# Optimization experiments

Measured on AMD Instinct MI355X. Metric: run time of the kernel, lower is better.

Reference implementation:

```python
import jax, jax.numpy as jnp
import numpy as np

N = 50000      # nodes
E = 800000     # edges
D_IN = 128     # raw feature dim
H = 96         # hidden_channels
K = 8          # experts
L = 4          # num_layers
C = 40         # classes


def setup_inputs() -> dict:
    key = jax.random.key(0)
    ks = jax.random.split(key, 10)
    stdv = 1.0 / np.sqrt(H)
    inp = {
        'x': jax.random.normal(ks[0], (N, D_IN), dtype=jnp.float32),
        'edge_index': jax.random.randint(ks[1], (2, E), 0, N, dtype=jnp.int64),
        # fcs[0]: Linear(d, hidden); fcs[1]: Linear(hidden, c)
        'fc0_w': jax.random.normal(ks[2], (D_IN, H), dtype=jnp.float32) * 0.05,
        'fc0_b': jnp.zeros((H,), dtype=jnp.float32),
        'fc1_w': jax.random.normal(ks[3], (H, C), dtype=jnp.float32) * 0.05,
        'fc1_b': jnp.zeros((C,), dtype=jnp.float32),
        # context_enc (method='node'): per-layer Linear(hidden, K)
        'ctx_w': jax.random.normal(ks[4], (L, H, K), dtype=jnp.float32) * 0.05,
        'ctx_b': jnp.zeros((L, K), dtype=jnp.float32),
        # GraphMultiConvolution weights: [L, K, hidden, hidden], uniform(-stdv, stdv)
        'conv_w': jax.random.uniform(ks[5], (L, K, H, H), dtype=jnp.float32,
                                     minval=-stdv, maxval=stdv),
    }
    return inp


def reference(x, edge_index, fc0_w, fc0_b, fc1_w, fc1_b, ctx_w, ctx_b, conv_w):
    # eval-mode forward (training=False): no dropout, softmax routing
    row = edge_index[0]
    col = edge_index[1]
    h = jax.nn.relu(x @ fc0_w + fc0_b)                     # [N, H]
    for i in range(L):
        # routing logits and soft expert weights z: [N, K]
        z = jax.nn.softmax(h @ ctx_w[i] + ctx_b[i], axis=-1)
        # spmm aggregation: hi[r] = sum over edges (r, c) of h[c]
        hi = jax.ops.segment_sum(h[col], row, num_segments=N)  # [N, H]
        # K-expert batched matmul: [N, K, H]
        outs = jnp.einsum('nd,kdo->nko', hi, conv_w[i])
        # gumbel/softmax-weighted combine + residual
        out = jnp.einsum('nk,nko->no', z, outs) + h
        h = jax.nn.relu(out)
    return h @ fc1_w + fc1_b                               # [N, C]
```

## Files before the change

### kernel.cpp

```cpp
#include <hip/hip_runtime.h>

#define N_NODES 50000
#define N_EDGES 800000
#define DIN     128
#define H       96
#define K_EXP   8
#define L_LAYERS 4
#define C_OUT   40

#define GSZ 6250

typedef _Float16 f16;
typedef f16 f16x2 __attribute__((ext_vector_type(2)));
typedef f16 f16x4 __attribute__((ext_vector_type(4)));
typedef f16 f16x8 __attribute__((ext_vector_type(8)));
typedef float f32x4 __attribute__((ext_vector_type(4)));


#define CONV_TOT (L_LAYERS * K_EXP * H * H)
#define FC0_TOT  (DIN * H)
#define FC1_TOT  (48 * H)
#define CNT_BLOCKS ((N_EDGES + 255) / 256)
#define CVT_BLOCKS ((CONV_TOT + FC0_TOT + FC1_TOT + 255) / 256)

__global__ __launch_bounds__(256) void count_convert(const int* __restrict__ row,
                                                     int* __restrict__ deg,
                                                     int* __restrict__ p,
                                                     const float* __restrict__ conv_w,
                                                     const float* __restrict__ fc0_w,
                                                     const float* __restrict__ fc1_w,
                                                     f16* __restrict__ wfrag,
                                                     f16* __restrict__ fc0t,
                                                     f16* __restrict__ fc1t) {
    int tid = threadIdx.x;
    if ((int)blockIdx.x < CNT_BLOCKS) {
        int i = blockIdx.x * 256 + tid;
        if (i < N_EDGES) p[i] = atomicAdd(&deg[row[i]], 1);
    } else {
        int i = ((int)blockIdx.x - CNT_BLOCKS) * 256 + tid;
        if (i < CONV_TOT) {
            int o = i % H;
            int t = i / H;
            int d = t % H;
            int lk = t / H;
            int ct = o >> 4, lc = o & 15;
            int ks = d >> 5, quad = (d >> 3) & 3, j = d & 7;
            wfrag[(size_t)lk * 9216 + ct * 1536 + ks * 512 + (quad * 16 + lc) * 8 + j] =
                (f16)conv_w[i];
        } else if (i < CONV_TOT + FC0_TOT) {
            int j = i - CONV_TOT;
            int o = j % H, d = j / H;
            fc0t[o * DIN + d] = (f16)fc0_w[j];
        } else if (i < CONV_TOT + FC0_TOT + FC1_TOT) {
            int j = i - CONV_TOT - FC0_TOT;
            int o = j / H, d = j % H;
            fc1t[j] = (o < C_OUT) ? (f16)fc1_w[d * C_OUT + o] : (f16)0.f;
        }
    }
}

__global__ __launch_bounds__(1024) void scanA(const int* __restrict__ deg,
                                              int* __restrict__ rowptr,
                                              int* __restrict__ partial, int n) {
    __shared__ int wsum[16];
    int tid  = threadIdx.x;
    int lane = tid & 63, wid = tid >> 6;
    int idx = blockIdx.x * 1024 + tid;
    int v = (idx < n) ? deg[idx] : 0;
    int s = v;
    #pragma unroll
    for (int off = 1; off < 64; off <<= 1) {
        int t = __shfl_up(s, off, 64);
        if (lane >= off) s += t;
    }
    if (lane == 63) wsum[wid] = s;
    __syncthreads();
    if (wid == 0 && lane < 16) {
        int w = wsum[lane];
        #pragma unroll
        for (int off = 1; off < 16; off <<= 1) {
            int t = __shfl_up(w, off, 16);
            if (lane >= off) w += t;
        }
        wsum[lane] = w;
    }
    __syncthreads();
    int waveoff = (wid == 0) ? 0 : wsum[wid - 1];
    if (idx < n) rowptr[idx + 1] = waveoff + s;
    if (tid == 1023) partial[blockIdx.x] = waveoff + s;
}

__global__ __launch_bounds__(1024) void scanC(int* __restrict__ rowptr,
                                              const int* __restrict__ partial,
                                              int nb, int n) {
    __shared__ int boff_s;
    int tid = threadIdx.x;
    if (tid < 64) {
        int v = 0;
        for (int j = tid; j < (int)blockIdx.x; j += 64) v += partial[j];
        #pragma unroll
        for (int off = 32; off >= 1; off >>= 1) v += __shfl_xor(v, off, 64);
        if (tid == 0) boff_s = v;
    }
    __syncthreads();
    int boff = boff_s;
    int idx = blockIdx.x * 1024 + tid;
    if (idx == 0) rowptr[0] = 0;
    if (idx < n) rowptr[idx + 1] += boff;
}

__global__ __launch_bounds__(256) void scatter_store_xcd(const int* __restrict__ row,
                                                         const int* __restrict__ col,
                                                         const int* __restrict__ p,
                                                         const int* __restrict__ rowptr,
                                                         int* __restrict__ csr, int e) {
    int g = blockIdx.x & 7;
    int rlo = g * GSZ, rhi = rlo + GSZ;
    int stride = (gridDim.x >> 3) * 256;
    for (int i = (blockIdx.x >> 3) * 256 + threadIdx.x; i < e; i += stride) {
        int r = row[i];
        if (r >= rlo && r < rhi)
            csr[rowptr[r] + p[i]] = col[i];
    }
}


#define SPMM_BLOCKS ((N_NODES + 15) / 16)
#define CTX_BLOCKS  ((N_NODES + 255) / 256)

#define ACC8(v) { _Pragma("unroll") for (int q = 0; q < 8; q++) acc[q] += (float)(v)[q]; }

__global__ __launch_bounds__(256) void layer_pre(const f16* __restrict__ h16,
                                                 const int* __restrict__ rowptr,
                                                 const int* __restrict__ csr,
                                                 f16* __restrict__ hi16,
                                                 const float* __restrict__ cw,
                                                 const float* __restrict__ cb,
                                                 float* __restrict__ zt, int n) {
    __shared__ float ws[H * K_EXP];
    __shared__ float bs[K_EXP];
    int tid = threadIdx.x;
    if ((int)blockIdx.x < SPMM_BLOCKS) {
        int r  = blockIdx.x * 16 + (tid >> 4);
        int li = tid & 15;
        if (r >= n) return;
        bool act = li < 12;
        int j = rowptr[r], e = rowptr[r + 1];
        float acc[8] = {};
        const f16* hb = h16 + li * 8;

        int4 qa = *(const int4*)(csr + j);
        int4 qb = *(const int4*)(csr + j + 4);

        while (j + 8 <= e) {
            int4 na = *(const int4*)(csr + j + 8);
            int4 nb = *(const int4*)(csr + j + 12);
            f16x8 v0 = {}, v1 = {}, v2 = {}, v3 = {}, v4 = {}, v5 = {}, v6 = {}, v7 = {};
            if (act) {
                v0 = *(const f16x8*)(hb + (size_t)qa.x * H);
                v1 = *(const f16x8*)(hb + (size_t)qa.y * H);
                v2 = *(const f16x8*)(hb + (size_t)qa.z * H);
                v3 = *(const f16x8*)(hb + (size_t)qa.w * H);
                v4 = *(const f16x8*)(hb + (size_t)qb.x * H);
                v5 = *(const f16x8*)(hb + (size_t)qb.y * H);
                v6 = *(const f16x8*)(hb + (size_t)qb.z * H);
                v7 = *(const f16x8*)(hb + (size_t)qb.w * H);
            }
            ACC8(v0) ACC8(v1) ACC8(v2) ACC8(v3)
            ACC8(v4) ACC8(v5) ACC8(v6) ACC8(v7)
            j += 8; qa = na; qb = nb;
        }
        if (j + 4 <= e) {
            f16x8 v0 = {}, v1 = {}, v2 = {}, v3 = {};
            if (act) {
                v0 = *(const f16x8*)(hb + (size_t)qa.x * H);
                v1 = *(const f16x8*)(hb + (size_t)qa.y * H);
                v2 = *(const f16x8*)(hb + (size_t)qa.z * H);
                v3 = *(const f16x8*)(hb + (size_t)qa.w * H);
            }
            ACC8(v0) ACC8(v1) ACC8(v2) ACC8(v3)
            j += 4; qa = qb;
        }
        int rem = e - j;
        if (rem > 0) {
            f16x8 v0 = {}, v1 = {}, v2 = {};
            if (act) {
                v0 = *(const f16x8*)(hb + (size_t)qa.x * H);
                if (rem > 1) v1 = *(const f16x8*)(hb + (size_t)qa.y * H);
                if (rem > 2) v2 = *(const f16x8*)(hb + (size_t)qa.z * H);
            }
            ACC8(v0)
            if (rem > 1) ACC8(v1)
            if (rem > 2) ACC8(v2)
        }
        if (act) {
            f16x8 o;
            #pragma unroll
            for (int q = 0; q < 8; q++) o[q] = (f16)acc[q];
            *(f16x8*)(hi16 + (size_t)r * H + li * 8) = o;
        }
    } else {
        for (int t = tid; t < H * K_EXP; t += 256) ws[t] = cw[t];
        if (tid < K_EXP) bs[tid] = cb[tid];
        __syncthreads();
        int node = ((int)blockIdx.x - SPMM_BLOCKS) * 256 + tid;
        if (node >= n) return;
        float acc[K_EXP];
        #pragma unroll
        for (int k = 0; k < K_EXP; k++) acc[k] = bs[k];
        const f16* hr = h16 + (size_t)node * H;
        #pragma unroll 3
        for (int c8 = 0; c8 < 12; c8++) {
            f16x8 v = *(const f16x8*)(hr + c8 * 8);
            #pragma unroll
            for (int j = 0; j < 8; j++) {
                float hv = (float)v[j];
                int d = c8 * 8 + j;
                #pragma unroll
                for (int k = 0; k < K_EXP; k++) acc[k] += hv * ws[d * K_EXP + k];
            }
        }
        float mx = acc[0];
        #pragma unroll
        for (int k = 1; k < K_EXP; k++) mx = fmaxf(mx, acc[k]);
        float s = 0.f;
        #pragma unroll
        for (int k = 0; k < K_EXP; k++) { acc[k] = __expf(acc[k] - mx); s += acc[k]; }
        float inv = 1.f / s;
        #pragma unroll
        for (int k = 0; k < K_EXP; k++)
            zt[(size_t)k * N_NODES + node] = acc[k] * inv;
    }
}


#define FPAD 136

__global__ __launch_bounds__(256) void fc0_kernel(const float* __restrict__ x,
                                                  const f16* __restrict__ fc0t,
                                                  const float* __restrict__ b,
                                                  f16* __restrict__ h16, int n) {
    __shared__ f16 As[64 * FPAD];
    __shared__ f16 Ws[96 * FPAD];
    int tid = threadIdx.x;
    int l = tid & 63, w = tid >> 6;
    int quad = l >> 4, lc = l & 15;
    int row0 = blockIdx.x * 64;

    for (int t = tid; t < 2048; t += 256) {
        int m = t >> 5, c4 = (t & 31) * 4;
        int gr = row0 + m;
        float4 v = {0.f, 0.f, 0.f, 0.f};
        if (gr < n) v = *(const float4*)(x + (size_t)gr * DIN + c4);
        f16x4 h4 = {(f16)v.x, (f16)v.y, (f16)v.z, (f16)v.w};
        *(f16x4*)&As[m * FPAD + c4] = h4;
    }
    for (int t = tid; t < 1536; t += 256) {
        int o = t >> 4, c8 = (t & 15) * 8;
        *(f16x8*)&Ws[o * FPAD + c8] = *(const f16x8*)(fc0t + o * DIN + c8);
    }
    __syncthreads();

    f16x8 afr[4];
    #pragma unroll
    for (int ks = 0; ks < 4; ks++)
        afr[ks] = *(const f16x8*)&As[(16 * w + lc) * FPAD + ks * 32 + quad * 8];

    f32x4 acc[6] = {};
    #pragma unroll
    for (int ct = 0; ct < 6; ct++) {
        #pragma unroll
        for (int ks = 0; ks < 4; ks++) {
            f16x8 bfr = *(const f16x8*)&Ws[(ct * 16 + lc) * FPAD + ks * 32 + quad * 8];
            acc[ct] = __builtin_amdgcn_mfma_f32_16x16x32_f16(afr[ks], bfr, acc[ct], 0, 0, 0);
        }
    }

    int m0 = 16 * w + quad * 4;
    #pragma unroll
    for (int r = 0; r < 4; r++) {
        int gr = row0 + m0 + r;
        if (gr < n) {
            #pragma unroll
            for (int ct = 0; ct < 6; ct++) {
                int o = ct * 16 + lc;
                h16[(size_t)gr * H + o] = (f16)fmaxf(acc[ct][r] + b[o], 0.f);
            }
        }
    }
}


#define EG_STAGE 2
#define EG_HALFS (EG_STAGE * 9216)

__global__ __launch_bounds__(256) void expert_gemm(const f16* __restrict__ hi16,
                                                   const f16* __restrict__ hin16,
                                                   const f16* __restrict__ wfrag,
                                                   const float* __restrict__ zt,
                                                   f16* __restrict__ hout16, int n) {
    __shared__ f16 Wl[EG_HALFS];
    int tid = threadIdx.x;
    int l = tid & 63, w = tid >> 6;
    int quad = l >> 4, lc = l & 15;
    int brow = blockIdx.x * 128;
    int wrow0 = brow + w * 16;
    int wrow1 = wrow0 + 64;

    f16x8 afr0[3], afr1[3];
    #pragma unroll
    for (int ks = 0; ks < 3; ks++) {
        afr0[ks] = *(const f16x8*)(hi16 + (size_t)(wrow0 + lc) * H + ks * 32 + quad * 8);
        afr1[ks] = *(const f16x8*)(hi16 + (size_t)(wrow1 + lc) * H + ks * 32 + quad * 8);
    }

    f32x4 acc0[6] = {};
    f32x4 acc1[6] = {};

    for (int kb = 0; kb < K_EXP; kb += EG_STAGE) {
        __syncthreads();
        const f16* src = wfrag + (size_t)kb * 9216;
        for (int t = tid; t < EG_HALFS / 8; t += 256)
            *(f16x8*)&Wl[t * 8] = *(const f16x8*)(src + t * 8);
        __syncthreads();

        #pragma unroll
        for (int k2 = 0; k2 < EG_STAGE; k2++) {
            int k = kb + k2;
            f32x4 zf0 = *(const f32x4*)(zt + (size_t)k * N_NODES + wrow0 + quad * 4);
            f32x4 zf1 = *(const f32x4*)(zt + (size_t)k * N_NODES + wrow1 + quad * 4);
            #pragma unroll
            for (int ct = 0; ct < 6; ct++) {
                f16x8 b0 = *(const f16x8*)&Wl[k2 * 9216 + ct * 1536 + 0 * 512 + l * 8];
                f16x8 b1 = *(const f16x8*)&Wl[k2 * 9216 + ct * 1536 + 1 * 512 + l * 8];
                f16x8 b2 = *(const f16x8*)&Wl[k2 * 9216 + ct * 1536 + 2 * 512 + l * 8];
                f32x4 t0 = {};
                t0 = __builtin_amdgcn_mfma_f32_16x16x32_f16(afr0[0], b0, t0, 0, 0, 0);
                t0 = __builtin_amdgcn_mfma_f32_16x16x32_f16(afr0[1], b1, t0, 0, 0, 0);
                t0 = __builtin_amdgcn_mfma_f32_16x16x32_f16(afr0[2], b2, t0, 0, 0, 0);
                acc0[ct] += zf0 * t0;
                f32x4 t1 = {};
                t1 = __builtin_amdgcn_mfma_f32_16x16x32_f16(afr1[0], b0, t1, 0, 0, 0);
                t1 = __builtin_amdgcn_mfma_f32_16x16x32_f16(afr1[1], b1, t1, 0, 0, 0);
                t1 = __builtin_amdgcn_mfma_f32_16x16x32_f16(afr1[2], b2, t1, 0, 0, 0);
                acc1[ct] += zf1 * t1;
            }
        }
    }

    #pragma unroll
    for (int r = 0; r < 4; r++) {
        int gr0 = wrow0 + quad * 4 + r;
        if (gr0 < n) {
            #pragma unroll
            for (int ct = 0; ct < 6; ct++) {
                int o = ct * 16 + lc;
                float v = fmaxf(acc0[ct][r] + (float)hin16[(size_t)gr0 * H + o], 0.f);
                hout16[(size_t)gr0 * H + o] = (f16)v;
            }
        }
        int gr1 = wrow1 + quad * 4 + r;
        if (gr1 < n) {
            #pragma unroll
            for (int ct = 0; ct < 6; ct++) {
                int o = ct * 16 + lc;
                float v = fmaxf(acc1[ct][r] + (float)hin16[(size_t)gr1 * H + o], 0.f);
                hout16[(size_t)gr1 * H + o] = (f16)v;
            }
        }
    }
}


#define APAD 104

__global__ __launch_bounds__(256) void fc1_kernel(const f16* __restrict__ h16,
                                                  const f16* __restrict__ fc1t,
                                                  const float* __restrict__ b,
                                                  float* __restrict__ out, int n) {
    __shared__ f16 As[64 * APAD];
    __shared__ f16 Ws[48 * APAD];
    int tid = threadIdx.x;
    int l = tid & 63, w = tid >> 6;
    int quad = l >> 4, lc = l & 15;
    int row0 = blockIdx.x * 64;

    for (int t = tid; t < 768; t += 256) {
        int m = t / 12, c8 = (t % 12) * 8;
        int gr = row0 + m;
        f16x8 v = {};
        if (gr < n) v = *(const f16x8*)(h16 + (size_t)gr * H + c8);
        *(f16x8*)&As[m * APAD + c8] = v;
    }
    for (int t = tid; t < 576; t += 256) {
        int o = t / 12, c8 = (t % 12) * 8;
        *(f16x8*)&Ws[o * APAD + c8] = *(const f16x8*)(fc1t + o * H + c8);
    }
    __syncthreads();

    f16x8 afr[3];
    #pragma unroll
    for (int ks = 0; ks < 3; ks++)
        afr[ks] = *(const f16x8*)&As[(16 * w + lc) * APAD + ks * 32 + quad * 8];

    f32x4 acc[3] = {};
    #pragma unroll
    for (int ct = 0; ct < 3; ct++) {
        #pragma unroll
        for (int ks = 0; ks < 3; ks++) {
            f16x8 bfr = *(const f16x8*)&Ws[(ct * 16 + lc) * APAD + ks * 32 + quad * 8];
            acc[ct] = __builtin_amdgcn_mfma_f32_16x16x32_f16(afr[ks], bfr, acc[ct], 0, 0, 0);
        }
    }

    int m0 = 16 * w + quad * 4;
    #pragma unroll
    for (int r = 0; r < 4; r++) {
        int gr = row0 + m0 + r;
        if (gr < n) {
            #pragma unroll
            for (int ct = 0; ct < 3; ct++) {
                int o = ct * 16 + lc;
                if (o < C_OUT)
                    out[(size_t)gr * C_OUT + o] = acc[ct][r] + b[o];
            }
        }
    }
}


extern "C" void kernel_launch(void* const* d_in, const int* in_sizes, int n_in,
                              void* d_out, int out_size, void* d_ws, size_t ws_size,
                              hipStream_t stream) {
    const float* x      = (const float*)d_in[0];
    const int*   ei     = (const int*)d_in[1];
    const float* fc0_w  = (const float*)d_in[2];
    const float* fc0_b  = (const float*)d_in[3];
    const float* fc1_w  = (const float*)d_in[4];
    const float* fc1_b  = (const float*)d_in[5];
    const float* ctx_w  = (const float*)d_in[6];
    const float* ctx_b  = (const float*)d_in[7];
    const float* conv_w = (const float*)d_in[8];
    float* out = (float*)d_out;

    const size_t NH = (size_t)N_NODES * H;

    float* zbuf = (float*)d_ws;
    f16*   h16a = (f16*)(zbuf + (size_t)N_NODES * K_EXP);
    f16*   h16b = h16a + NH;
    f16*   hi16 = h16b + NH;
    f16*   wfrag= hi16 + NH;
    f16*   fc0t = wfrag + CONV_TOT;
    f16*   fc1t = fc0t + FC0_TOT;
    int* rowptr = (int*)(fc1t + FC1_TOT);
    int* deg    = rowptr + (N_NODES + 1);
    int* csr    = deg + N_NODES;
    int* prank  = csr + N_EDGES;
    int* partial  = prank + N_EDGES;

    const int* row = ei;
    const int* col = ei + N_EDGES;

    hipMemsetAsync(deg, 0, sizeof(int) * N_NODES, stream);

    count_convert<<<CNT_BLOCKS + CVT_BLOCKS, 256, 0, stream>>>(
        row, deg, prank, conv_w, fc0_w, fc1_w, wfrag, fc0t, fc1t);
    int nsb = (N_NODES + 1023) / 1024;
    scanA<<<nsb, 1024, 0, stream>>>(deg, rowptr, partial, N_NODES);
    scanC<<<nsb, 1024, 0, stream>>>(rowptr, partial, nsb, N_NODES);
    scatter_store_xcd<<<1024, 256, 0, stream>>>(row, col, prank, rowptr, csr, N_EDGES);

    int gemm_grid = (N_NODES + 63) / 64;
    fc0_kernel<<<gemm_grid, 256, 0, stream>>>(x, fc0t, fc0_b, h16a, N_NODES);

    int eg_grid = (N_NODES + 127) / 128;
    f16* hcur = h16a;
    f16* hnext = h16b;
    for (int i = 0; i < L_LAYERS; i++) {
        layer_pre<<<SPMM_BLOCKS + CTX_BLOCKS, 256, 0, stream>>>(
            hcur, rowptr, csr, hi16,
            ctx_w + (size_t)i * H * K_EXP, ctx_b + (size_t)i * K_EXP, zbuf, N_NODES);
        expert_gemm<<<eg_grid, 256, 0, stream>>>(
            hi16, hcur, wfrag + (size_t)i * K_EXP * H * H, zbuf, hnext, N_NODES);
        f16* t = hcur; hcur = hnext; hnext = t;
    }
    fc1_kernel<<<gemm_grid, 256, 0, stream>>>(hcur, fc1t, fc1_b, out, N_NODES);
}
```

Measured before the change: 369.7 us.

## Fuse CSR scatter with fc0, fold routing weights into A operand of expert MFMA

```diff
diff --git a/kernel.cpp b/kernel.cpp
--- a/kernel.cpp
+++ b/kernel.cpp
@@ -7,8 +7,6 @@
 #define K_EXP   8
 #define L_LAYERS 4
 #define C_OUT   40
-
-#define GSZ 6250
 
 typedef _Float16 f16;
 typedef f16 f16x2 __attribute__((ext_vector_type(2)));
@@ -109,18 +107,72 @@
     if (idx < n) rowptr[idx + 1] += boff;
 }
 
-__global__ __launch_bounds__(256) void scatter_store_xcd(const int* __restrict__ row,
-                                                         const int* __restrict__ col,
-                                                         const int* __restrict__ p,
-                                                         const int* __restrict__ rowptr,
-                                                         int* __restrict__ csr, int e) {
-    int g = blockIdx.x & 7;
-    int rlo = g * GSZ, rhi = rlo + GSZ;
-    int stride = (gridDim.x >> 3) * 256;
-    for (int i = (blockIdx.x >> 3) * 256 + threadIdx.x; i < e; i += stride) {
-        int r = row[i];
-        if (r >= rlo && r < rhi)
-            csr[rowptr[r] + p[i]] = col[i];
+
+#define SCT_BLOCKS 1024
+#define FPAD 136
+
+__global__ __launch_bounds__(256) void scatter_fc0(const int* __restrict__ row,
+                                                   const int* __restrict__ col,
+                                                   const int* __restrict__ p,
+                                                   const int* __restrict__ rowptr,
+                                                   int* __restrict__ csr,
+                                                   const float* __restrict__ x,
+                                                   const f16* __restrict__ fc0t,
+                                                   const float* __restrict__ b,
+                                                   f16* __restrict__ h16, int n) {
+    __shared__ f16 As[64 * FPAD];
+    __shared__ f16 Ws[96 * FPAD];
+    int tid = threadIdx.x;
+    if ((int)blockIdx.x < SCT_BLOCKS) {
+        int stride = SCT_BLOCKS * 256;
+        for (int i = blockIdx.x * 256 + tid; i < N_EDGES; i += stride)
+            csr[rowptr[row[i]] + p[i]] = col[i];
+        return;
+    }
+    int l = tid & 63, w = tid >> 6;
+    int quad = l >> 4, lc = l & 15;
+    int row0 = ((int)blockIdx.x - SCT_BLOCKS) * 64;
+
+    for (int t = tid; t < 2048; t += 256) {
+        int m = t >> 5, c4 = (t & 31) * 4;
+        int gr = row0 + m;
+        float4 v = {0.f, 0.f, 0.f, 0.f};
+        if (gr < n) v = *(const float4*)(x + (size_t)gr * DIN + c4);
+        f16x4 h4 = {(f16)v.x, (f16)v.y, (f16)v.z, (f16)v.w};
+        *(f16x4*)&As[m * FPAD + c4] = h4;
+    }
+    for (int t = tid; t < 1536; t += 256) {
+        int o = t >> 4, c8 = (t & 15) * 8;
+        *(f16x8*)&Ws[o * FPAD + c8] = *(const f16x8*)(fc0t + o * DIN + c8);
+    }
+    __syncthreads();
+
+    f16x8 afr[4];
+    #pragma unroll
+    for (int ks = 0; ks < 4; ks++)
+        afr[ks] = *(const f16x8*)&As[(16 * w + lc) * FPAD + ks * 32 + quad * 8];
+
+    f32x4 acc[6] = {};
+    #pragma unroll
+    for (int ct = 0; ct < 6; ct++) {
+        #pragma unroll
+        for (int ks = 0; ks < 4; ks++) {
+            f16x8 bfr = *(const f16x8*)&Ws[(ct * 16 + lc) * FPAD + ks * 32 + quad * 8];
+            acc[ct] = __builtin_amdgcn_mfma_f32_16x16x32_f16(afr[ks], bfr, acc[ct], 0, 0, 0);
+        }
+    }
+
+    int m0 = 16 * w + quad * 4;
+    #pragma unroll
+    for (int r = 0; r < 4; r++) {
+        int gr = row0 + m0 + r;
+        if (gr < n) {
+            #pragma unroll
+            for (int ct = 0; ct < 6; ct++) {
+                int o = ct * 16 + lc;
+                h16[(size_t)gr * H + o] = (f16)fmaxf(acc[ct][r] + b[o], 0.f);
+            }
+        }
     }
 }
 
@@ -227,66 +279,10 @@
         #pragma unroll
         for (int k = 0; k < K_EXP; k++) { acc[k] = __expf(acc[k] - mx); s += acc[k]; }
         float inv = 1.f / s;
-        #pragma unroll
-        for (int k = 0; k < K_EXP; k++)
-            zt[(size_t)k * N_NODES + node] = acc[k] * inv;
-    }
-}
-
-
-#define FPAD 136
-
-__global__ __launch_bounds__(256) void fc0_kernel(const float* __restrict__ x,
-                                                  const f16* __restrict__ fc0t,
-                                                  const float* __restrict__ b,
-                                                  f16* __restrict__ h16, int n) {
-    __shared__ f16 As[64 * FPAD];
-    __shared__ f16 Ws[96 * FPAD];
-    int tid = threadIdx.x;
-    int l = tid & 63, w = tid >> 6;
-    int quad = l >> 4, lc = l & 15;
-    int row0 = blockIdx.x * 64;
-
-    for (int t = tid; t < 2048; t += 256) {
-        int m = t >> 5, c4 = (t & 31) * 4;
-        int gr = row0 + m;
-        float4 v = {0.f, 0.f, 0.f, 0.f};
-        if (gr < n) v = *(const float4*)(x + (size_t)gr * DIN + c4);
-        f16x4 h4 = {(f16)v.x, (f16)v.y, (f16)v.z, (f16)v.w};
-        *(f16x4*)&As[m * FPAD + c4] = h4;
-    }
-    for (int t = tid; t < 1536; t += 256) {
-        int o = t >> 4, c8 = (t & 15) * 8;
-        *(f16x8*)&Ws[o * FPAD + c8] = *(const f16x8*)(fc0t + o * DIN + c8);
-    }
-    __syncthreads();
-
-    f16x8 afr[4];
-    #pragma unroll
-    for (int ks = 0; ks < 4; ks++)
-        afr[ks] = *(const f16x8*)&As[(16 * w + lc) * FPAD + ks * 32 + quad * 8];
-
-    f32x4 acc[6] = {};
-    #pragma unroll
-    for (int ct = 0; ct < 6; ct++) {
-        #pragma unroll
-        for (int ks = 0; ks < 4; ks++) {
-            f16x8 bfr = *(const f16x8*)&Ws[(ct * 16 + lc) * FPAD + ks * 32 + quad * 8];
-            acc[ct] = __builtin_amdgcn_mfma_f32_16x16x32_f16(afr[ks], bfr, acc[ct], 0, 0, 0);
-        }
-    }
-
-    int m0 = 16 * w + quad * 4;
-    #pragma unroll
-    for (int r = 0; r < 4; r++) {
-        int gr = row0 + m0 + r;
-        if (gr < n) {
-            #pragma unroll
-            for (int ct = 0; ct < 6; ct++) {
-                int o = ct * 16 + lc;
-                h16[(size_t)gr * H + o] = (f16)fmaxf(acc[ct][r] + b[o], 0.f);
-            }
-        }
+        f32x4 za = {acc[0] * inv, acc[1] * inv, acc[2] * inv, acc[3] * inv};
+        f32x4 zb = {acc[4] * inv, acc[5] * inv, acc[6] * inv, acc[7] * inv};
+        *(f32x4*)(zt + (size_t)node * K_EXP) = za;
+        *(f32x4*)(zt + (size_t)node * K_EXP + 4) = zb;
     }
 }
 
@@ -314,6 +310,17 @@
         afr1[ks] = *(const f16x8*)(hi16 + (size_t)(wrow1 + lc) * H + ks * 32 + quad * 8);
     }
 
+    f32x4 z0a = *(const f32x4*)(zt + (size_t)(wrow0 + lc) * K_EXP);
+    f32x4 z0b = *(const f32x4*)(zt + (size_t)(wrow0 + lc) * K_EXP + 4);
+    f32x4 z1a = *(const f32x4*)(zt + (size_t)(wrow1 + lc) * K_EXP);
+    f32x4 z1b = *(const f32x4*)(zt + (size_t)(wrow1 + lc) * K_EXP + 4);
+    f16 zh0[K_EXP], zh1[K_EXP];
+    #pragma unroll
+    for (int k = 0; k < 4; k++) {
+        zh0[k] = (f16)z0a[k]; zh0[k + 4] = (f16)z0b[k];
+        zh1[k] = (f16)z1a[k]; zh1[k + 4] = (f16)z1b[k];
+    }
+
     f32x4 acc0[6] = {};
     f32x4 acc1[6] = {};
 
@@ -327,23 +334,24 @@
         #pragma unroll
         for (int k2 = 0; k2 < EG_STAGE; k2++) {
             int k = kb + k2;
-            f32x4 zf0 = *(const f32x4*)(zt + (size_t)k * N_NODES + wrow0 + quad * 4);
-            f32x4 zf1 = *(const f32x4*)(zt + (size_t)k * N_NODES + wrow1 + quad * 4);
+            f16 s0 = zh0[k], s1 = zh1[k];
+            f16x8 a0s[3], a1s[3];
+            #pragma unroll
+            for (int ks = 0; ks < 3; ks++) {
+                a0s[ks] = afr0[ks] * s0;
+                a1s[ks] = afr1[ks] * s1;
+            }
             #pragma unroll
             for (int ct = 0; ct < 6; ct++) {
                 f16x8 b0 = *(const f16x8*)&Wl[k2 * 9216 + ct * 1536 + 0 * 512 + l * 8];
                 f16x8 b1 = *(const f16x8*)&Wl[k2 * 9216 + ct * 1536 + 1 * 512 + l * 8];
                 f16x8 b2 = *(const f16x8*)&Wl[k2 * 9216 + ct * 1536 + 2 * 512 + l * 8];
-                f32x4 t0 = {};
-                t0 = __builtin_amdgcn_mfma_f32_16x16x32_f16(afr0[0], b0, t0, 0, 0, 0);
-                t0 = __builtin_amdgcn_mfma_f32_16x16x32_f16(afr0[1], b1, t0, 0, 0, 0);
-                t0 = __builtin_amdgcn_mfma_f32_16x16x32_f16(afr0[2], b2, t0, 0, 0, 0);
-                acc0[ct] += zf0 * t0;
-                f32x4 t1 = {};
-                t1 = __builtin_amdgcn_mfma_f32_16x16x32_f16(afr1[0], b0, t1, 0, 0, 0);
-                t1 = __builtin_amdgcn_mfma_f32_16x16x32_f16(afr1[1], b1, t1, 0, 0, 0);
-                t1 = __builtin_amdgcn_mfma_f32_16x16x32_f16(afr1[2], b2, t1, 0, 0, 0);
-                acc1[ct] += zf1 * t1;
+                acc0[ct] = __builtin_amdgcn_mfma_f32_16x16x32_f16(a0s[0], b0, acc0[ct], 0, 0, 0);
+                acc0[ct] = __builtin_amdgcn_mfma_f32_16x16x32_f16(a0s[1], b1, acc0[ct], 0, 0, 0);
+                acc0[ct] = __builtin_amdgcn_mfma_f32_16x16x32_f16(a0s[2], b2, acc0[ct], 0, 0, 0);
+                acc1[ct] = __builtin_amdgcn_mfma_f32_16x16x32_f16(a1s[0], b0, acc1[ct], 0, 0, 0);
+                acc1[ct] = __builtin_amdgcn_mfma_f32_16x16x32_f16(a1s[1], b1, acc1[ct], 0, 0, 0);
+                acc1[ct] = __builtin_amdgcn_mfma_f32_16x16x32_f16(a1s[2], b2, acc1[ct], 0, 0, 0);
             }
         }
     }
@@ -468,10 +476,10 @@
     int nsb = (N_NODES + 1023) / 1024;
     scanA<<<nsb, 1024, 0, stream>>>(deg, rowptr, partial, N_NODES);
     scanC<<<nsb, 1024, 0, stream>>>(rowptr, partial, nsb, N_NODES);
-    scatter_store_xcd<<<1024, 256, 0, stream>>>(row, col, prank, rowptr, csr, N_EDGES);
 
     int gemm_grid = (N_NODES + 63) / 64;
-    fc0_kernel<<<gemm_grid, 256, 0, stream>>>(x, fc0t, fc0_b, h16a, N_NODES);
+    scatter_fc0<<<SCT_BLOCKS + gemm_grid, 256, 0, stream>>>(
+        row, col, prank, rowptr, csr, x, fc0t, fc0_b, h16a, N_NODES);
 
     int eg_grid = (N_NODES + 127) / 128;
     f16* hcur = h16a;
```

Result: faster. 350.6 us (-5.2%).
